# Optimization experiments

Measured on AMD Instinct MI355X. Metric: run time of the kernel, lower is better.

Reference implementation:

```python
import jax, jax.numpy as jnp
import numpy as np

NF, IN_NF, N_LAYERS = 64, 196, 3
B, H, W = 1, 256, 256
P3 = [(1, 1), (1, 1)]
P1 = [(0, 0), (0, 0)]


def conv2d(x, w, pad):
    return jax.lax.conv_general_dilated(x, w, (1, 1), pad,
                                        dimension_numbers=('NCHW', 'OIHW', 'NCHW'))


def prelu(x, a):
    return jnp.where(x >= 0, x, a[None, :, None, None] * x)


def warp(x, flow):
    # standard backward bilinear warp, zero padding outside the image
    Bx, C, Hx, Wx = x.shape
    yy, xx = jnp.meshgrid(jnp.arange(Hx, dtype=x.dtype),
                          jnp.arange(Wx, dtype=x.dtype), indexing='ij')
    px = xx[None] + flow[:, 0]  # (B,H,W)
    py = yy[None] + flow[:, 1]

    def sample(img, px, py):  # img (C,H,W); px,py (H,W)
        x0 = jnp.floor(px)
        y0 = jnp.floor(py)
        x1 = x0 + 1.0
        y1 = y0 + 1.0
        wx1 = px - x0
        wx0 = 1.0 - wx1
        wy1 = py - y0
        wy0 = 1.0 - wy1

        def gather(xi, yi):
            valid = (xi >= 0) & (xi <= Wx - 1) & (yi >= 0) & (yi <= Hx - 1)
            xc = jnp.clip(xi, 0, Wx - 1).astype(jnp.int32)
            yc = jnp.clip(yi, 0, Hx - 1).astype(jnp.int32)
            return img[:, yc, xc] * valid.astype(img.dtype)

        return (gather(x0, y0) * (wx0 * wy0) + gather(x1, y0) * (wx1 * wy0)
                + gather(x0, y1) * (wx0 * wy1) + gather(x1, y1) * (wx1 * wy1))

    return jax.vmap(sample)(x, px, py)


def setup_inputs() -> dict:
    key = jax.random.key(0)
    ks = jax.random.split(key, 11)
    s = 0.05
    return {
        'feat_0': jax.random.normal(ks[0], (B, 64, H, W), jnp.float32),
        'feat_1': jax.random.normal(ks[1], (B, 64, H, W), jnp.float32),
        'feat_dense': jax.random.normal(ks[2], (B, 64, H, W), jnp.float32),
        'flow': jax.random.normal(ks[3], (B, 4, H, W), jnp.float32),
        'space_mask': jax.random.uniform(ks[4], (B, 1, H, W), jnp.float32),
        'head_w': jax.random.normal(ks[5], (IN_NF, IN_NF, 3, 3), jnp.float32) * s,
        'head_a': jnp.full((IN_NF,), 0.25, jnp.float32),
        'conv_w': jax.random.normal(ks[6], (N_LAYERS, IN_NF, IN_NF, 3, 3), jnp.float32) * s,
        'conv_a': jnp.full((N_LAYERS, IN_NF), 0.25, jnp.float32),
        'last_w': jax.random.normal(ks[7], (4 + NF, IN_NF * (N_LAYERS + 1), 1, 1), jnp.float32) * s,
        'last_b': jax.random.normal(ks[8], (4 + NF,), jnp.float32) * s,
        'mask_w': jax.random.normal(ks[9], (2, NF, 3, 3), jnp.float32) * s,
        'mask_b': jax.random.normal(ks[10], (2,), jnp.float32) * s,
    }


def reference(feat_0, feat_1, feat_dense, flow, space_mask,
              head_w, head_a, conv_w, conv_a, last_w, last_b, mask_w, mask_b):
    f0 = warp(feat_0, flow[:, :2])
    f1 = warp(feat_1, flow[:, 2:4])
    x = jnp.concatenate([f0, f1, feat_dense, flow], axis=1)  # (B, in_nf, H, W)
    sm_up = jnp.repeat(jnp.repeat(space_mask, 2, axis=2), 2, axis=3)

    # head: conv3x3 -> PReLU, then mask (dense / use_sparsity=False path)
    x = prelu(conv2d(x, head_w, P3), head_a) * space_mask
    outs = [x]
    for i in range(N_LAYERS):
        x = conv2d(x, conv_w[i], P3) * space_mask
        x = prelu(x, conv_a[i])
        outs.append(x)
    x = conv2d(jnp.concatenate(outs, axis=1), last_w, P1) + last_b[None, :, None, None]

    smn = conv2d(x[:, 4:], mask_w, P3) + mask_b[None, :, None, None]

    Bx, Cx, Hx, Wx = x.shape
    x_up = jax.image.resize(x, (Bx, Cx, 2 * Hx, 2 * Wx), method='bilinear')
    smn_up = jax.image.resize(smn, (Bx, 2, 2 * Hx, 2 * Wx), method='bilinear')

    flow_out = x_up[:, :4]
    feat_t = x_up[:, 4:]
    # eval-mode mask (training=False): hard argmax between channel 0 and 1
    mask_next = (smn_up[:, :1] > smn_up[:, 1:2]).astype(x.dtype) * sm_up
    return flow_out, feat_t, mask_next
```

## Files before the change

kernel.cpp:

```cpp
#include <hip/hip_runtime.h>

typedef _Float16 f16;
typedef _Float16 f16x8 __attribute__((ext_vector_type(8)));
typedef _Float16 f16x4 __attribute__((ext_vector_type(4)));
typedef float    f32x4 __attribute__((ext_vector_type(4)));
typedef float    f32x16 __attribute__((ext_vector_type(16)));

#define MFMA16(a,b,c) __builtin_amdgcn_mfma_f32_16x16x32_f16(a,b,c,0,0,0)
#define MFMA32(a,b,c) __builtin_amdgcn_mfma_f32_32x32x16_f16(a,b,c,0,0,0)

#define AS1 __attribute__((address_space(1)))
#define AS3 __attribute__((address_space(3)))

#define NPIX 65536
#define PXS   8
#define KHS   2064
#define K16S  4128
#define HS    8256
#define CBS   16512
#define ROWH  115584
#define RBYTES 231168
#define SBUF  ((size_t)258*RBYTES)

#define PKSUB  7168
#define PK_CONV 903168
#define NMICRO 117

#define PKL_CB  5120
#define PKL_BI  35840

#define ASTG 14336

__global__ void k_pack_conv(const float* __restrict__ head_w,
                            const float* __restrict__ conv_w,
                            f16* __restrict__ dst)
{
    int t = blockIdx.x*256 + threadIdx.x;
    int lane = t & 63; t >>= 6;
    int ob  = t % 7;  t /= 7;
    int sel = t & 1;  t >>= 1;
    int kx  = t % 3;  t /= 3;
    int k16 = t & 1;  t >>= 1;
    int cb  = t % 7;  t /= 7;
    int ky  = t % 3;  t /= 3;
    int li  = t;
    if (li >= 4) return;
    if (cb == 6 && k16 == 1) return;
    const float* W = (li == 0) ? head_w : (conv_w + (size_t)(li-1)*196*196*9);
    int oc  = ob*32 + (lane & 31);
    int ic0 = cb*32 + k16*16 + (lane >> 5)*8;
    int tap = ky*3 + kx;
    f16x8 v;
#pragma unroll
    for (int j = 0; j < 8; ++j) {
        int ic = ic0 + j;
        float x = 0.f;
        if (oc < 196 && ic < 196) x = W[((size_t)oc*196 + ic)*9 + tap];
        f16 h = (f16)x;
        v[j] = (sel == 0) ? h : (f16)(x - (float)h);
    }
    int pos = ky*39 + ((cb < 6) ? (cb*6 + k16*3 + kx) : (36 + kx));
    *(f16x8*)(dst + (size_t)li*PK_CONV + (size_t)pos*PKSUB
              + (size_t)(sel*7 + ob)*512 + (size_t)lane*8) = v;
}

__global__ void k_pack_last(const float* __restrict__ last_w, f16* __restrict__ dst)
{
    int t = blockIdx.x*256 + threadIdx.x;
    if (t >= 4*7*5*2*64) return;
    int lane = t & 63; t >>= 6;
    int sel  = t & 1;  t >>= 1;
    int ob   = t % 5;  t /= 5;
    int cb   = t % 7;  t /= 7;
    int bi   = t;
    int oc = ob*16 + (lane & 15);
    int k0 = cb*32 + (lane >> 4)*8;
    f16x8 v;
#pragma unroll
    for (int j = 0; j < 8; ++j) {
        int k = k0 + j;
        float x = 0.f;
        if (oc < 68 && k < 196) x = last_w[(size_t)oc*784 + bi*196 + k];
        f16 h = (f16)x;
        v[j] = (sel == 0) ? h : (f16)(x - (float)h);
    }
    *(f16x8*)(dst + (((size_t)((bi*7+cb)*5 + ob)*2 + sel)*64 + lane)*8) = v;
}

__global__ void k_zero_halo(f16* __restrict__ bufA, f16* __restrict__ bufB)
{
    int c = blockIdx.x*256 + threadIdx.x;
    int end = c & 1; c >>= 1;
    int kh  = c & 1; c >>= 1;
    int k16 = c & 1; c >>= 1;
    int h   = c & 1; c >>= 1;
    int cb  = c % 7; c /= 7;
    int row = c % 258; c /= 258;
    if (c >= 2) return;
    f16* base = (c == 0) ? bufA : bufB;
    f16* p = base + (size_t)row*ROWH + cb*CBS + h*HS + k16*K16S + kh*KHS + (end ? 257 : 0)*PXS;
    f16x8 z = {(f16)0,(f16)0,(f16)0,(f16)0,(f16)0,(f16)0,(f16)0,(f16)0};
    *(f16x8*)p = z;
}

struct Gath { int o00,o01,o10,o11; float w00,w01,w10,w11; };

__device__ inline Gath mk_gath(float pxf, float pyf)
{
    float x0 = floorf(pxf), y0 = floorf(pyf);
    float x1 = x0 + 1.f, y1 = y0 + 1.f;
    float wx1 = pxf - x0, wx0 = 1.f - wx1;
    float wy1 = pyf - y0, wy0 = 1.f - wy1;
    bool vx0 = (x0 >= 0.f) && (x0 <= 255.f);
    bool vx1 = (x1 >= 0.f) && (x1 <= 255.f);
    bool vy0 = (y0 >= 0.f) && (y0 <= 255.f);
    bool vy1 = (y1 >= 0.f) && (y1 <= 255.f);
    int ix0 = min(max((int)x0, 0), 255);
    int ix1 = min(max((int)x1, 0), 255);
    int iy0 = min(max((int)y0, 0), 255);
    int iy1 = min(max((int)y1, 0), 255);
    Gath g;
    g.o00 = iy0*256 + ix0; g.w00 = (vx0 && vy0) ? wx0*wy0 : 0.f;
    g.o01 = iy0*256 + ix1; g.w01 = (vx1 && vy0) ? wx1*wy0 : 0.f;
    g.o10 = iy1*256 + ix0; g.w10 = (vx0 && vy1) ? wx0*wy1 : 0.f;
    g.o11 = iy1*256 + ix1; g.w11 = (vx1 && vy1) ? wx1*wy1 : 0.f;
    return g;
}

__device__ inline void store4n(f16* __restrict__ rowb, int slot, int c0,
                               float a, float b, float c, float d)
{
    f16x4 hi, lo;
    f16 h;
    h = (f16)a; hi[0] = h; lo[0] = (f16)(a - (float)h);
    h = (f16)b; hi[1] = h; lo[1] = (f16)(b - (float)h);
    h = (f16)c; hi[2] = h; lo[2] = (f16)(c - (float)h);
    h = (f16)d; hi[3] = h; lo[3] = (f16)(d - (float)h);
    int cb = c0 >> 5, w32 = c0 & 31;
    f16* p = rowb + cb*CBS + (w32 >> 4)*K16S + ((w32 >> 3) & 1)*KHS
                 + (size_t)slot*PXS + (w32 & 7);
    *(f16x4*)p        = hi;
    *(f16x4*)(p + HS) = lo;
}

__global__ void k_warp_concat(const float* __restrict__ f0, const float* __restrict__ f1,
                              const float* __restrict__ fd, const float* __restrict__ flow,
                              f16* __restrict__ out)
{
    int px = blockIdx.x*256 + threadIdx.x;
    int row = px >> 8, col = px & 255;
    f16* rowb = out + (size_t)(row+1)*ROWH;
    int slot = col + 1;
    Gath g0 = mk_gath((float)col + flow[px],          (float)row + flow[NPIX   + px]);
    Gath g1 = mk_gath((float)col + flow[2*NPIX + px], (float)row + flow[3*NPIX + px]);
#pragma unroll
    for (int c = 0; c < 64; c += 4) {
        float v[4];
#pragma unroll
        for (int r = 0; r < 4; ++r) {
            const float* im = f0 + (size_t)(c+r)*NPIX;
            v[r] = g0.w00*im[g0.o00] + g0.w01*im[g0.o01] + g0.w10*im[g0.o10] + g0.w11*im[g0.o11];
        }
        store4n(rowb, slot, c, v[0], v[1], v[2], v[3]);
    }
#pragma unroll
    for (int c = 0; c < 64; c += 4) {
        float v[4];
#pragma unroll
        for (int r = 0; r < 4; ++r) {
            const float* im = f1 + (size_t)(c+r)*NPIX;
            v[r] = g1.w00*im[g1.o00] + g1.w01*im[g1.o01] + g1.w10*im[g1.o10] + g1.w11*im[g1.o11];
        }
        store4n(rowb, slot, 64 + c, v[0], v[1], v[2], v[3]);
    }
#pragma unroll
    for (int c = 0; c < 64; c += 4) {
        store4n(rowb, slot, 128 + c, fd[(size_t)(c+0)*NPIX + px], fd[(size_t)(c+1)*NPIX + px],
                                     fd[(size_t)(c+2)*NPIX + px], fd[(size_t)(c+3)*NPIX + px]);
    }
    store4n(rowb, slot, 192, flow[px], flow[NPIX+px], flow[2*NPIX+px], flow[3*NPIX+px]);
#pragma unroll
    for (int c = 196; c < 224; c += 4) store4n(rowb, slot, c, 0.f, 0.f, 0.f, 0.f);
}

__global__ __launch_bounds__(256, 2)
void k_conv32(const f16* __restrict__ in, f16* __restrict__ out,
              const f16* __restrict__ pack, const float* __restrict__ alpha,
              const float* __restrict__ mask)
{
    __shared__ __align__(16) char As[2][ASTG];

    int bid = blockIdx.x;
    int wg  = (bid & 7)*64 + (bid >> 3);
    int row  = wg >> 1;
    int half = wg & 1;
    int tid  = threadIdx.x;
    int lane = tid & 63;
    int w    = tid >> 6;
    int pxt  = half*4 + w;
    int l31 = lane & 31, lk = lane >> 5;

    f32x16 acc[7];
#pragma unroll
    for (int o = 0; o < 7; ++o)
#pragma unroll
        for (int e = 0; e < 16; ++e) acc[o][e] = 0.f;

    auto stage = [&](int b, const f16* src) {
        __builtin_amdgcn_global_load_lds(
            (const AS1 void*)(src + (size_t)tid*8),
            (AS3 void*)(&As[b][0] + tid*16), 16, 0, 0);
        __builtin_amdgcn_global_load_lds(
            (const AS1 void*)(src + (size_t)(tid+256)*8),
            (AS3 void*)(&As[b][0] + (tid+256)*16), 16, 0, 0);
        __builtin_amdgcn_global_load_lds(
            (const AS1 void*)(src + (size_t)(tid+512)*8),
            (AS3 void*)(&As[b][0] + (tid+512)*16), 16, 0, 0);
        if (tid < 128)
            __builtin_amdgcn_global_load_lds(
                (const AS1 void*)(src + (size_t)(tid+768)*8),
                (AS3 void*)(&As[b][0] + (tid+768)*16), 16, 0, 0);
    };

    auto lB = [&](const f16* bp, f16x8& H, f16x8& L) {
        H = *(const f16x8*)bp;
        L = *(const f16x8*)(bp + HS);
    };

    const f16* bcol = in + (size_t)lk*KHS + (size_t)(pxt*32 + l31)*PXS;

    f16x8 Bh0, Bl0, Bh1, Bl1;
    stage(0, pack);
    lB(bcol + (size_t)row*ROWH, Bh0, Bl0);
    __syncthreads();

    int bsel = 0, q = 0;
    for (int ky = 0; ky < 3; ++ky) {
        const f16* brow = bcol + (size_t)(row + ky)*ROWH;
        for (int cb = 0; cb < 7; ++cb) {
            const f16* bcb = brow + cb*CBS;
            const f16* bnext = (cb < 6) ? (bcb + CBS) : (brow + ROWH);
            int nk16 = (cb == 6) ? 1 : 2;
            for (int k16 = 0; k16 < 2; ++k16) {
                if (k16 >= nk16) break;
#pragma unroll
                for (int kx = 0; kx < 3; ++kx) {
                    bool last = (q == NMICRO - 1);
                    if (!last) {
                        stage(bsel ^ 1, pack + (size_t)(q+1)*PKSUB);
                        const f16* nb;
                        if (kx < 2)                  nb = bcb + k16*K16S + (kx+1)*PXS;
                        else if (k16 == 0 && cb < 6) nb = bcb + K16S;
                        else                         nb = bnext;
                        lB(nb, Bh1, Bl1);
                    }
                    const char* ab = &As[bsel][0];
                    __builtin_amdgcn_s_setprio(1);
#pragma unroll
                    for (int o = 0; o < 7; ++o) {
                        f16x8 Ah = *(const f16x8*)(ab + o*1024 + lane*16);
                        f16x8 Al = *(const f16x8*)(ab + (7+o)*1024 + lane*16);
                        acc[o] = MFMA32(Ah, Bh0, acc[o]);
                        acc[o] = MFMA32(Al, Bh0, acc[o]);
                        acc[o] = MFMA32(Ah, Bl0, acc[o]);
                    }
                    __builtin_amdgcn_s_setprio(0);
                    __syncthreads();
                    bsel ^= 1; ++q;
                    Bh0 = Bh1; Bl0 = Bl1;
                }
            }
        }
    }

    float mv = mask[row*256 + pxt*32 + l31];
    f16* orow = out + (size_t)(row+1)*ROWH + (size_t)(pxt*32 + l31 + 1)*PXS + lk*4;
#pragma unroll
    for (int o = 0; o < 7; ++o) {
#pragma unroll
        for (int qg = 0; qg < 4; ++qg) {
            int oc0 = o*32 + 8*qg + 4*lk;
            f32x4 a4 = *(const f32x4*)(alpha + min(oc0, 192));
            f16x4 hi, lo;
#pragma unroll
            for (int e = 0; e < 4; ++e) {
                float v = acc[o][qg*4 + e];
                v = (v >= 0.f ? v : a4[e]*v) * mv;
                f16 h = (f16)v;
                hi[e] = h;
                lo[e] = (f16)(v - (float)h);
            }
            f16* p = orow + o*CBS + (qg >> 1)*K16S + (qg & 1)*KHS;
            *(f16x4*)p        = hi;
            *(f16x4*)(p + HS) = lo;
        }
    }
}

__global__ __launch_bounds__(256, 4)
void k_acc_last(const f16* __restrict__ in, const f16* __restrict__ pack,
                const float* __restrict__ bias, float* __restrict__ accp, int bi)
{
    int lane = threadIdx.x & 63;
    int wid  = (blockIdx.x << 2) | (threadIdx.x >> 6);
    int row  = wid >> 3;
    int col0 = (wid & 7) << 5;
    int l15 = lane & 15, lk = lane >> 4;

    f32x4 acc[5][2];
#pragma unroll
    for (int i = 0; i < 5; ++i)
#pragma unroll
        for (int j = 0; j < 2; ++j)
            acc[i][j] = (f32x4){0.f, 0.f, 0.f, 0.f};

    const f16* bb = in + (size_t)(row+1)*ROWH + (size_t)(col0 + l15 + 1)*PXS
                  + (lk >> 1)*K16S + (lk & 1)*KHS;
    const f16* ap = pack + (size_t)bi*PKL_BI + (size_t)lane*8;
    for (int cb = 0; cb < 7; ++cb) {
        f16x8 bh[2], bl[2];
#pragma unroll
        for (int pb = 0; pb < 2; ++pb) {
            const f16* p = bb + cb*CBS + pb*16*PXS;
            bh[pb] = *(const f16x8*)p;
            bl[pb] = *(const f16x8*)(p + HS);
        }
        const f16* a = ap + cb*PKL_CB;
#pragma unroll
        for (int ob = 0; ob < 5; ++ob) {
            f16x8 ah = *(const f16x8*)(a + ob*1024);
            f16x8 al = *(const f16x8*)(a + ob*1024 + 512);
#pragma unroll
            for (int pb = 0; pb < 2; ++pb) {
                acc[ob][pb] = MFMA16(ah, bh[pb], acc[ob][pb]);
                acc[ob][pb] = MFMA16(ah, bl[pb], acc[ob][pb]);
                acc[ob][pb] = MFMA16(al, bh[pb], acc[ob][pb]);
            }
        }
    }
#pragma unroll
    for (int ob = 0; ob < 5; ++ob) {
        int oc0 = ob*16 + lk*4;
        if (oc0 >= 72) continue;
#pragma unroll
        for (int pb = 0; pb < 2; ++pb) {
            int px = row*256 + col0 + pb*16 + l15;
            float* dst = accp + (size_t)px*72 + oc0;
            f32x4 d = acc[ob][pb];
            if (bi == 0) {
                f32x4 b4;
#pragma unroll
                for (int r = 0; r < 4; ++r) b4[r] = bias[min(oc0 + r, 67)];
                *(f32x4*)dst = d + b4;
            } else {
                *(f32x4*)dst = *(const f32x4*)dst + d;
            }
        }
    }
}

__global__ void k_smn(const float* __restrict__ accp, const float* __restrict__ mw,
                      const float* __restrict__ mb, float* __restrict__ smn)
{
    int px = blockIdx.x*256 + threadIdx.x;
    int row = px >> 8, col = px & 255;
    float s0 = mb[0], s1 = mb[1];
    for (int ky = 0; ky < 3; ++ky) {
        int r = row + ky - 1;
        if ((unsigned)r > 255u) continue;
        for (int kx = 0; kx < 3; ++kx) {
            int c = col + kx - 1;
            if ((unsigned)c > 255u) continue;
            const float* ab = accp + ((size_t)r*256 + c)*72 + 4;
            const float* w  = mw + ky*3 + kx;
#pragma unroll
            for (int ch = 0; ch < 64; ch += 4) {
                f32x4 v = *(const f32x4*)(ab + ch);
                s0 += v[0]*w[(ch+0)*9] + v[1]*w[(ch+1)*9] + v[2]*w[(ch+2)*9] + v[3]*w[(ch+3)*9];
                s1 += v[0]*w[(64+ch+0)*9] + v[1]*w[(64+ch+1)*9] + v[2]*w[(64+ch+2)*9] + v[3]*w[(64+ch+3)*9];
            }
        }
    }
    smn[px]        = s0;
    smn[NPIX + px] = s1;
}

__global__ void k_up(const float* __restrict__ accp, const float* __restrict__ smn,
                     const float* __restrict__ sm, float* __restrict__ outp)
{
    int o = blockIdx.x*256 + threadIdx.x;
    int oy = o >> 9, ox = o & 511;
    int my = oy >> 1, mx = ox >> 1;
    int r0, r1, c0, c1; float wy0, wy1, wx0, wx1;
    if (oy & 1) { r0 = my;            r1 = min(my+1, 255); wy0 = 0.75f; wy1 = 0.25f; }
    else        { r0 = max(my-1, 0);  r1 = my;             wy0 = 0.25f; wy1 = 0.75f; }
    if (ox & 1) { c0 = mx;            c1 = min(mx+1, 255); wx0 = 0.75f; wx1 = 0.25f; }
    else        { c0 = max(mx-1, 0);  c1 = mx;             wx0 = 0.25f; wx1 = 0.75f; }
    float w00 = wy0*wx0, w01 = wy0*wx1, w10 = wy1*wx0, w11 = wy1*wx1;
    int i00 = r0*256 + c0, i01 = r0*256 + c1, i10 = r1*256 + c0, i11 = r1*256 + c1;

    const float* p00 = accp + (size_t)i00*72;
    const float* p01 = accp + (size_t)i01*72;
    const float* p10 = accp + (size_t)i10*72;
    const float* p11 = accp + (size_t)i11*72;
#pragma unroll
    for (int ch = 0; ch < 68; ch += 4) {
        f32x4 va = *(const f32x4*)(p00 + ch);
        f32x4 vb = *(const f32x4*)(p01 + ch);
        f32x4 vc = *(const f32x4*)(p10 + ch);
        f32x4 vd = *(const f32x4*)(p11 + ch);
        f32x4 v;
#pragma unroll
        for (int r = 0; r < 4; ++r)
            v[r] = w00*va[r] + w01*vb[r] + w10*vc[r] + w11*vd[r];
        outp[(size_t)(ch+0)*262144 + o] = v[0];
        outp[(size_t)(ch+1)*262144 + o] = v[1];
        outp[(size_t)(ch+2)*262144 + o] = v[2];
        outp[(size_t)(ch+3)*262144 + o] = v[3];
    }
    float s0 = w00*smn[i00] + w01*smn[i01] + w10*smn[i10] + w11*smn[i11];
    float s1 = w00*smn[NPIX+i00] + w01*smn[NPIX+i01] + w10*smn[NPIX+i10] + w11*smn[NPIX+i11];
    outp[(size_t)68*262144 + o] = (s0 > s1) ? sm[my*256 + mx] : 0.f;
}

extern "C" void kernel_launch(void* const* d_in, const int* in_sizes, int n_in,
                              void* d_out, int out_size, void* d_ws, size_t ws_size,
                              hipStream_t stream)
{
    const float* feat0  = (const float*)d_in[0];
    const float* feat1  = (const float*)d_in[1];
    const float* featd  = (const float*)d_in[2];
    const float* flow   = (const float*)d_in[3];
    const float* smask  = (const float*)d_in[4];
    const float* head_w = (const float*)d_in[5];
    const float* head_a = (const float*)d_in[6];
    const float* conv_w = (const float*)d_in[7];
    const float* conv_a = (const float*)d_in[8];
    const float* last_w = (const float*)d_in[9];
    const float* last_b = (const float*)d_in[10];
    const float* mask_w = (const float*)d_in[11];
    const float* mask_b = (const float*)d_in[12];
    float* outp = (float*)d_out;

    char* ws = (char*)d_ws;
    size_t off = 0;
    f16* bufA = (f16*)(ws + off); off += SBUF;
    f16* bufB = (f16*)(ws + off); off += SBUF;
    f16* packc = (f16*)(ws + off); off += (size_t)4*PK_CONV*2;
    f16* packl = (f16*)(ws + off); off += (size_t)4*PKL_BI*2;
    float* accp = (float*)(ws + off); off += (size_t)NPIX*72*4;
    float* smn  = (float*)(ws + off); off += (size_t)2*NPIX*4;

    hipMemsetAsync(bufA, 0, RBYTES, stream);
    hipMemsetAsync((char*)bufA + (size_t)257*RBYTES, 0, RBYTES, stream);
    hipMemsetAsync(bufB, 0, RBYTES, stream);
    hipMemsetAsync((char*)bufB + (size_t)257*RBYTES, 0, RBYTES, stream);
    k_zero_halo<<<226, 256, 0, stream>>>(bufA, bufB);

    k_pack_conv<<<1764, 256, 0, stream>>>(head_w, conv_w, packc);
    k_pack_last<<<70, 256, 0, stream>>>(last_w, packl);
    k_warp_concat<<<256, 256, 0, stream>>>(feat0, feat1, featd, flow, bufA);

    k_conv32<<<512, 256, 0, stream>>>(bufA, bufB, packc, head_a, smask);
    k_acc_last<<<512, 256, 0, stream>>>(bufB, packl, last_b, accp, 0);
    k_conv32<<<512, 256, 0, stream>>>(bufB, bufA, packc + (size_t)1*PK_CONV, conv_a, smask);
    k_acc_last<<<512, 256, 0, stream>>>(bufA, packl, last_b, accp, 1);
    k_conv32<<<512, 256, 0, stream>>>(bufA, bufB, packc + (size_t)2*PK_CONV, conv_a + 196, smask);
    k_acc_last<<<512, 256, 0, stream>>>(bufB, packl, last_b, accp, 2);
    k_conv32<<<512, 256, 0, stream>>>(bufB, bufA, packc + (size_t)3*PK_CONV, conv_a + 392, smask);
    k_acc_last<<<512, 256, 0, stream>>>(bufA, packl, last_b, accp, 3);

    k_smn<<<256, 256, 0, stream>>>(accp, mask_w, mask_b, smn);
    k_up<<<1024, 256, 0, stream>>>(accp, smn, smask, outp);
}
```

Measured before the change: 774.9 us.

## Triple-buffer weight staging and prefetch next A fragments into registers

Expands the LDS weight staging from double to triple buffering, issuing the async global-to-LDS copy two micro-steps ahead. The high-half A fragments for the next step are preloaded into registers before the current MFMA block, so that LDS read latency is hidden behind compute. This adds LDS usage and about 28 extra VGPRs of live register state. That could reduce occupancy or cause spills under the two-blocks-per-CU launch bound.

New measurement: 783.9 us. No clear change (+1.2%).

```diff
diff --git a/kernel.cpp b/kernel.cpp
--- a/kernel.cpp
+++ b/kernel.cpp
@@ -188,7 +188,7 @@
               const f16* __restrict__ pack, const float* __restrict__ alpha,
               const float* __restrict__ mask)
 {
-    __shared__ __align__(16) char As[2][ASTG];
+    __shared__ __align__(16) char As[3][ASTG];
 
     int bid = blockIdx.x;
     int wg  = (bid & 7)*64 + (bid >> 3);
@@ -231,10 +231,16 @@
 
     f16x8 Bh0, Bl0, Bh1, Bl1;
     stage(0, pack);
+    stage(1, pack + PKSUB);
     lB(bcol + (size_t)row*ROWH, Bh0, Bl0);
     __syncthreads();
 
-    int bsel = 0, q = 0;
+    f16x8 AhR[7];
+#pragma unroll
+    for (int o = 0; o < 7; ++o)
+        AhR[o] = *(const f16x8*)(&As[0][0] + o*1024 + lane*16);
+
+    int acur = 0, q = 0;
     for (int ky = 0; ky < 3; ++ky) {
         const f16* brow = bcol + (size_t)(row + ky)*ROWH;
         for (int cb = 0; cb < 7; ++cb) {
@@ -246,28 +252,39 @@
 #pragma unroll
                 for (int kx = 0; kx < 3; ++kx) {
                     bool last = (q == NMICRO - 1);
+                    int anx = (acur == 2) ? 0 : (acur + 1);
+                    if (q + 2 < NMICRO) {
+                        int ast = (anx == 2) ? 0 : (anx + 1);
+                        stage(ast, pack + (size_t)(q+2)*PKSUB);
+                    }
+                    f16x8 AhN[7];
                     if (!last) {
-                        stage(bsel ^ 1, pack + (size_t)(q+1)*PKSUB);
                         const f16* nb;
                         if (kx < 2)                  nb = bcb + k16*K16S + (kx+1)*PXS;
                         else if (k16 == 0 && cb < 6) nb = bcb + K16S;
                         else                         nb = bnext;
                         lB(nb, Bh1, Bl1);
+#pragma unroll
+                        for (int o = 0; o < 7; ++o)
+                            AhN[o] = *(const f16x8*)(&As[anx][0] + o*1024 + lane*16);
                     }
-                    const char* ab = &As[bsel][0];
+                    const char* ab = &As[acur][0];
                     __builtin_amdgcn_s_setprio(1);
 #pragma unroll
                     for (int o = 0; o < 7; ++o) {
-                        f16x8 Ah = *(const f16x8*)(ab + o*1024 + lane*16);
                         f16x8 Al = *(const f16x8*)(ab + (7+o)*1024 + lane*16);
-                        acc[o] = MFMA32(Ah, Bh0, acc[o]);
+                        acc[o] = MFMA32(AhR[o], Bh0, acc[o]);
                         acc[o] = MFMA32(Al, Bh0, acc[o]);
-                        acc[o] = MFMA32(Ah, Bl0, acc[o]);
+                        acc[o] = MFMA32(AhR[o], Bl0, acc[o]);
                     }
                     __builtin_amdgcn_s_setprio(0);
                     __syncthreads();
-                    bsel ^= 1; ++q;
-                    Bh0 = Bh1; Bl0 = Bl1;
+                    if (!last) {
+#pragma unroll
+                        for (int o = 0; o < 7; ++o) AhR[o] = AhN[o];
+                        Bh0 = Bh1; Bl0 = Bl1;
+                    }
+                    acur = anx; ++q;
                 }
             }
         }
```

## Fuse 1x1 last-conv partial accumulation into following 3x3 conv kernel

Applied to the files above, without the earlier changes.

The 1x1 last-layer contribution of each intermediate activation is now computed inside the next 3x3 conv kernel, reusing the center-tap (ky=1,kx=1) B fragments already loaded. This removes three separate k_acc_last launches and their full re-read of the activation buffer. A new packing kernel lays out last_w for 32x32 MFMA tiles. The cost is extra accumulator registers (3 more f32x16) in an already register-heavy kernel, which may hurt occupancy, plus extra global loads of A fragments on center-tap iterations.

Result: faster. 745.6 us, median of 2 (-3.8%).

```diff
diff --git a/kernel.cpp b/kernel.cpp
--- a/kernel.cpp
+++ b/kernel.cpp
@@ -28,6 +28,8 @@
 
 #define PKL_CB  5120
 #define PKL_BI  35840
+#define PK1_S   3072
+#define PK1_BI  39936
 
 #define ASTG 14336
 
@@ -85,6 +87,32 @@
         v[j] = (sel == 0) ? h : (f16)(x - (float)h);
     }
     *(f16x8*)(dst + (((size_t)((bi*7+cb)*5 + ob)*2 + sel)*64 + lane)*8) = v;
+}
+
+__global__ void k_pack_last32(const float* __restrict__ last_w, f16* __restrict__ dst)
+{
+    int t = blockIdx.x*256 + threadIdx.x;
+    if (t >= 4*13*2*3*64) return;
+    int lane = t & 63; t >>= 6;
+    int ob   = t % 3;  t /= 3;
+    int sel  = t & 1;  t >>= 1;
+    int s    = t % 13; t /= 13;
+    int bi   = t;
+    int cb  = (s < 12) ? (s >> 1) : 6;
+    int k16 = (s < 12) ? (s & 1)  : 0;
+    int oc  = ob*32 + (lane & 31);
+    int ic0 = cb*32 + k16*16 + (lane >> 5)*8;
+    f16x8 v;
+#pragma unroll
+    for (int j = 0; j < 8; ++j) {
+        int ic = ic0 + j;
+        float x = 0.f;
+        if (oc < 68 && ic < 196) x = last_w[(size_t)oc*784 + bi*196 + ic];
+        f16 h = (f16)x;
+        v[j] = (sel == 0) ? h : (f16)(x - (float)h);
+    }
+    *(f16x8*)(dst + (size_t)bi*PK1_BI + (size_t)s*PK1_S
+              + (size_t)(sel*3 + ob)*512 + (size_t)lane*8) = v;
 }
 
 __global__ void k_zero_halo(f16* __restrict__ bufA, f16* __restrict__ bufB)
@@ -186,7 +214,8 @@
 __global__ __launch_bounds__(256, 2)
 void k_conv32(const f16* __restrict__ in, f16* __restrict__ out,
               const f16* __restrict__ pack, const float* __restrict__ alpha,
-              const float* __restrict__ mask)
+              const float* __restrict__ mask, const f16* __restrict__ pk1,
+              const float* __restrict__ bias1, float* __restrict__ accp, int bi1)
 {
     __shared__ __align__(16) char As[2][ASTG];
 
@@ -205,6 +234,11 @@
     for (int o = 0; o < 7; ++o)
 #pragma unroll
         for (int e = 0; e < 16; ++e) acc[o][e] = 0.f;
+    f32x16 acc1[3];
+#pragma unroll
+    for (int o = 0; o < 3; ++o)
+#pragma unroll
+        for (int e = 0; e < 16; ++e) acc1[o][e] = 0.f;
 
     auto stage = [&](int b, const f16* src) {
         __builtin_amdgcn_global_load_lds(
@@ -254,6 +288,18 @@
                         else                         nb = bnext;
                         lB(nb, Bh1, Bl1);
                     }
+                    bool ctr = (ky == 1) && (kx == 1) && (bi1 >= 0);
+                    f16x8 A1h[3], A1l[3];
+                    if (ctr) {
+                        int s = (cb < 6) ? (cb*2 + k16) : 12;
+                        const f16* a1 = pk1 + (size_t)bi1*PK1_BI + (size_t)s*PK1_S
+                                      + (size_t)lane*8;
+#pragma unroll
+                        for (int o = 0; o < 3; ++o) {
+                            A1h[o] = *(const f16x8*)(a1 + o*512);
+                            A1l[o] = *(const f16x8*)(a1 + (3+o)*512);
+                        }
+                    }
                     const char* ab = &As[bsel][0];
                     __builtin_amdgcn_s_setprio(1);
 #pragma unroll
@@ -263,6 +309,14 @@
                         acc[o] = MFMA32(Ah, Bh0, acc[o]);
                         acc[o] = MFMA32(Al, Bh0, acc[o]);
                         acc[o] = MFMA32(Ah, Bl0, acc[o]);
+                    }
+                    if (ctr) {
+#pragma unroll
+                        for (int o = 0; o < 3; ++o) {
+                            acc1[o] = MFMA32(A1h[o], Bh0, acc1[o]);
+                            acc1[o] = MFMA32(A1l[o], Bh0, acc1[o]);
+                            acc1[o] = MFMA32(A1h[o], Bl0, acc1[o]);
+                        }
                     }
                     __builtin_amdgcn_s_setprio(0);
                     __syncthreads();
@@ -295,6 +349,29 @@
             *(f16x4*)(p + HS) = lo;
         }
     }
+    if (bi1 >= 0) {
+        int px = row*256 + pxt*32 + l31;
+        float* dst = accp + (size_t)px*72;
+#pragma unroll
+        for (int o = 0; o < 3; ++o) {
+#pragma unroll
+            for (int qg = 0; qg < 4; ++qg) {
+                int oc0 = o*32 + 8*qg + 4*lk;
+                if (oc0 >= 72) continue;
+                f32x4 d;
+#pragma unroll
+                for (int e = 0; e < 4; ++e) d[e] = acc1[o][qg*4 + e];
+                if (bi1 == 0) {
+                    f32x4 b4;
+#pragma unroll
+                    for (int e = 0; e < 4; ++e) b4[e] = bias1[min(oc0 + e, 67)];
+                    *(f32x4*)(dst + oc0) = d + b4;
+                } else {
+                    *(f32x4*)(dst + oc0) = *(const f32x4*)(dst + oc0) + d;
+                }
+            }
+        }
+    }
 }
 
 __global__ __launch_bounds__(256, 4)
@@ -346,15 +423,7 @@
         for (int pb = 0; pb < 2; ++pb) {
             int px = row*256 + col0 + pb*16 + l15;
             float* dst = accp + (size_t)px*72 + oc0;
-            f32x4 d = acc[ob][pb];
-            if (bi == 0) {
-                f32x4 b4;
-#pragma unroll
-                for (int r = 0; r < 4; ++r) b4[r] = bias[min(oc0 + r, 67)];
-                *(f32x4*)dst = d + b4;
-            } else {
-                *(f32x4*)dst = *(const f32x4*)dst + d;
-            }
+            *(f32x4*)dst = *(const f32x4*)dst + acc[ob][pb];
         }
     }
 }
@@ -448,6 +517,7 @@
     f16* bufB = (f16*)(ws + off); off += SBUF;
     f16* packc = (f16*)(ws + off); off += (size_t)4*PK_CONV*2;
     f16* packl = (f16*)(ws + off); off += (size_t)4*PKL_BI*2;
+    f16* pack1 = (f16*)(ws + off); off += (size_t)4*PK1_BI*2;
     float* accp = (float*)(ws + off); off += (size_t)NPIX*72*4;
     float* smn  = (float*)(ws + off); off += (size_t)2*NPIX*4;
 
@@ -459,15 +529,17 @@
 
     k_pack_conv<<<1764, 256, 0, stream>>>(head_w, conv_w, packc);
     k_pack_last<<<70, 256, 0, stream>>>(last_w, packl);
+    k_pack_last32<<<78, 256, 0, stream>>>(last_w, pack1);
     k_warp_concat<<<256, 256, 0, stream>>>(feat0, feat1, featd, flow, bufA);
 
-    k_conv32<<<512, 256, 0, stream>>>(bufA, bufB, packc, head_a, smask);
-    k_acc_last<<<512, 256, 0, stream>>>(bufB, packl, last_b, accp, 0);
-    k_conv32<<<512, 256, 0, stream>>>(bufB, bufA, packc + (size_t)1*PK_CONV, conv_a, smask);
-    k_acc_last<<<512, 256, 0, stream>>>(bufA, packl, last_b, accp, 1);
-    k_conv32<<<512, 256, 0, stream>>>(bufA, bufB, packc + (size_t)2*PK_CONV, conv_a + 196, smask);
-    k_acc_last<<<512, 256, 0, stream>>>(bufB, packl, last_b, accp, 2);
-    k_conv32<<<512, 256, 0, stream>>>(bufB, bufA, packc + (size_t)3*PK_CONV, conv_a + 392, smask);
+    k_conv32<<<512, 256, 0, stream>>>(bufA, bufB, packc, head_a, smask,
+                                      pack1, last_b, accp, -1);
+    k_conv32<<<512, 256, 0, stream>>>(bufB, bufA, packc + (size_t)1*PK_CONV, conv_a, smask,
+                                      pack1, last_b, accp, 0);
+    k_conv32<<<512, 256, 0, stream>>>(bufA, bufB, packc + (size_t)2*PK_CONV, conv_a + 196, smask,
+                                      pack1, last_b, accp, 1);
+    k_conv32<<<512, 256, 0, stream>>>(bufB, bufA, packc + (size_t)3*PK_CONV, conv_a + 392, smask,
+                                      pack1, last_b, accp, 2);
     k_acc_last<<<512, 256, 0, stream>>>(bufA, packl, last_b, accp, 3);
 
     k_smn<<<256, 256, 0, stream>>>(accp, mask_w, mask_b, smn);
```
